# Performance work log

Measured on AMD Instinct MI355X. Metric: run time of the kernel, lower is better.

## Reference

```python
import jax, jax.numpy as jnp
import numpy as np

# Grid config derived from module constants:
# point_cloud_range=[0,-25.6,-2,51.2,25.6,4.4], occ_size=[256,256,32], lss_downsample=[2,2,2]
DX = jnp.array([0.4, 0.4, 0.4], dtype=jnp.float32)
BX = jnp.array([0.2, -25.4, -1.8], dtype=jnp.float32)
NX = (128, 128, 16)  # (x, y, z) voxel counts


def setup_inputs() -> dict:
    key = jax.random.key(0)
    k1, k2, k3 = jax.random.split(key, 3)
    B, N, D, H, W, C = 2, 1, 40, 64, 128, 64  # fH=grd_h//4, fW=grd_w//4, D=40 depth bins
    img_feats = jax.random.normal(k1, (B * N, C, H, W), dtype=jnp.float32)
    depth_logits = jax.random.normal(k2, (B * N, D, H, W), dtype=jnp.float32)
    lo = jnp.array([0.0, -25.6, -2.0], dtype=jnp.float32)
    hi = jnp.array([51.2, 25.6, 4.4], dtype=jnp.float32)
    u = jax.random.uniform(k3, (B, N, D, H, W, 3), dtype=jnp.float32)
    geom = lo + u * (hi - lo)  # ego-frame 3D points of each frustum cell
    return {"img_feats": img_feats, "depth_logits": depth_logits, "geom": geom}


def reference(img_feats, depth_logits, geom):
    B, N, D, H, W, _ = geom.shape
    C = img_feats.shape[1]
    nx_x, nx_y, nx_z = NX

    # ---- LSS lift: depth-distribution-weighted outer product ----
    depth = jax.nn.softmax(depth_logits, axis=1)               # [BN, D, H, W]
    lifted = depth[:, None] * img_feats[:, :, None]            # [BN, C, D, H, W]
    x = lifted.reshape(B, N, C, D, H, W).transpose(0, 1, 3, 4, 5, 2)  # [B,N,D,H,W,C]

    # ---- voxel pooling (splat): scatter-add into BEV/3D grid ----
    Nprime = B * N * D * H * W
    xf = x.reshape(Nprime, C)
    coords = jnp.floor((geom.reshape(Nprime, 3) - (BX - DX / 2.0)) / DX).astype(jnp.int32)
    batch_ix = jnp.repeat(jnp.arange(B, dtype=jnp.int32), N * D * H * W)

    nx_arr = jnp.array(NX, dtype=jnp.int32)
    kept = jnp.all((coords >= 0) & (coords < nx_arr), axis=1)  # in-grid mask

    # linear index: ((b*Z + z)*X + x)*Y + y  -> grid layout [B, Z, X, Y]
    lin = ((batch_ix * nx_z + coords[:, 2]) * nx_x + coords[:, 0]) * nx_y + coords[:, 1]
    lin = jnp.where(kept, lin, 0)
    xf = jnp.where(kept[:, None], xf, 0.0)

    pooled = jax.ops.segment_sum(xf, lin, num_segments=B * nx_z * nx_x * nx_y)  # [B*Z*X*Y, C]

    # final grid [B, C, Z, X, Y]; cat(unbind(dim=2), 1) -> [B, Z*C, X, Y]
    final = pooled.reshape(B, nx_z, nx_x, nx_y, C).transpose(0, 1, 4, 2, 3)  # [B, Z, C, X, Y]
    out = final.reshape(B, nx_z * C, nx_x, nx_y)
    return out
```

## Files before the change

kernel.cpp:

```cpp
#include <hip/hip_runtime.h>
#include <cstddef>

#define BB 2
#define NN 1
#define DD 40
#define HH 64
#define WW 128
#define CC 64
#define GX 128
#define GY 128
#define GZ 16
#define XY (GX * GY)
#define VOX (BB * GZ * GX * GY)
#define KSLOT 16

__global__ __launch_bounds__(256) void lss_tfeat(
    const float* __restrict__ img, float* __restrict__ featT,
    uint4* __restrict__ count4) {
  __shared__ float tile[64][65];
  const int bn = blockIdx.x >> 7;
  const int p0 = (blockIdx.x & 127) << 6;
  const int t = threadIdx.x;

  {
    int base = blockIdx.x * 512 + t;
    count4[base] = make_uint4(0, 0, 0, 0);
    count4[base + 256] = make_uint4(0, 0, 0, 0);
  }

  const float* src = img + (size_t)bn * CC * (HH * WW);
#pragma unroll
  for (int i = 0; i < 4; ++i) {
    int idx = i * 256 + t;
    int r = idx >> 4;
    int c4 = idx & 15;
    float4 v = *(const float4*)(src + (size_t)r * (HH * WW) + p0 + c4 * 4);
    tile[r][c4 * 4 + 0] = v.x;
    tile[r][c4 * 4 + 1] = v.y;
    tile[r][c4 * 4 + 2] = v.z;
    tile[r][c4 * 4 + 3] = v.w;
  }
  __syncthreads();
  float* dst = featT + ((size_t)bn * (HH * WW) + p0) * CC;
#pragma unroll
  for (int i = 0; i < 4; ++i) {
    int idx = i * 256 + t;
    int p = idx >> 4;
    int q = idx & 15;
    float4 v;
    v.x = tile[q * 4 + 0][p];
    v.y = tile[q * 4 + 1][p];
    v.z = tile[q * 4 + 2][p];
    v.w = tile[q * 4 + 3][p];
    *(float4*)(dst + (size_t)p * CC + q * 4) = v;
  }
}

__global__ __launch_bounds__(64) void lss_bin(
    const float* __restrict__ logits, const float* __restrict__ geom,
    unsigned int* __restrict__ count, uint2* __restrict__ rec) {
  const int t = threadIdx.x;
  const int pix = blockIdx.x * 64 + t;
  const int w = pix & (WW - 1);
  const int h = (pix >> 7) & (HH - 1);
  const int bn = pix >> 13;

  float lg[DD];
  const float* lp = logits + ((size_t)bn * DD * HH + h) * WW + w;
#pragma unroll
  for (int d = 0; d < DD; ++d) lg[d] = lp[(size_t)d * (HH * WW)];

  float m = lg[0];
#pragma unroll
  for (int d = 1; d < DD; ++d) m = fmaxf(m, lg[d]);
  float s = 0.0f;
#pragma unroll
  for (int d = 0; d < DD; ++d) {
    lg[d] = __expf(lg[d] - m);
    s += lg[d];
  }
  const float inv = 1.0f / s;

  const float* gp = geom + ((size_t)(bn * DD * HH + h) * WW + w) * 3;
#pragma unroll 8
  for (int d = 0; d < DD; ++d) {
    const size_t gb = (size_t)d * (HH * WW * 3);
    float gx = gp[gb + 0];
    float gy = gp[gb + 1];
    float gz = gp[gb + 2];
    int cx = (int)floorf((gx - 0.0f) / 0.4f);
    int cy = (int)floorf((gy + 25.6f) / 0.4f);
    int cz = (int)floorf((gz + 2.0f) / 0.4f);
    if (cx >= 0 && cx < GX && cy >= 0 && cy < GY && cz >= 0 && cz < GZ) {
      int b = bn / NN;
      int v = ((b * GZ + cz) * GX + cx) * GY + cy;
      unsigned int slot = atomicAdd(&count[v], 1u);
      if (slot < KSLOT)
        rec[(size_t)slot * VOX + v] =
            make_uint2((unsigned)pix, __float_as_uint(lg[d] * inv));
    }
  }
}

__global__ __launch_bounds__(256) void lss_gather(
    const unsigned int* __restrict__ count, const uint2* __restrict__ rec,
    const float* __restrict__ featT, float* __restrict__ out) {
  __shared__ float accs[CC][65];
  __shared__ uint2 recs[KSLOT][64];
  __shared__ unsigned int cnts[64];
  const int t = threadIdx.x;
  const int v0 = blockIdx.x << 6;

  if (t < 64) {
    unsigned int c = count[v0 + t];
    cnts[t] = c > KSLOT ? KSLOT : c;
  }
  __syncthreads();

  {
    const int y = t & 63;
    const int cn = (int)cnts[y];
    for (int s = (t >> 6); s < KSLOT; s += 4)
      if (s < cn) recs[s][y] = rec[(size_t)s * VOX + v0 + y];
  }
  __syncthreads();

  const int lane = t & 63;
  const int wid = t >> 6;
  const int y0 = wid * 16;

  float a[16];
  int cn[16];
#pragma unroll
  for (int i = 0; i < 16; ++i) {
    a[i] = 0.0f;
    cn[i] = (int)cnts[y0 + i];
  }
  int maxcn = 0;
#pragma unroll
  for (int i = 0; i < 16; ++i) maxcn = cn[i] > maxcn ? cn[i] : maxcn;

  for (int s = 0; s < maxcn; ++s) {
    float f[16], w[16];
#pragma unroll
    for (int i = 0; i < 16; ++i) {
      if (s < cn[i]) {
        uint2 r = recs[s][y0 + i];
        w[i] = __uint_as_float(r.y);
        f[i] = featT[(size_t)r.x * CC + lane];
      }
    }
#pragma unroll
    for (int i = 0; i < 16; ++i)
      if (s < cn[i]) a[i] += w[i] * f[i];
  }

#pragma unroll
  for (int i = 0; i < 16; ++i) accs[lane][y0 + i] = a[i];
  __syncthreads();

  const int slab = v0 >> 14;
  const int xy = v0 & (XY - 1);
#pragma unroll
  for (int pass = 0; pass < 4; ++pass) {
    const int c = pass * 16 + (t >> 4);
    const int q = t & 15;
    float4 v;
    v.x = accs[c][q * 4 + 0];
    v.y = accs[c][q * 4 + 1];
    v.z = accs[c][q * 4 + 2];
    v.w = accs[c][q * 4 + 3];
    *(float4*)(out + ((size_t)slab * CC + c) * XY + xy + q * 4) = v;
  }
}

__global__ __launch_bounds__(256) void lss_scatter_direct(
    const float* __restrict__ img, const float* __restrict__ logits,
    const float* __restrict__ geom, float* __restrict__ acc) {
  const int gtid = blockIdx.x * blockDim.x + threadIdx.x;
  const int pix = gtid >> 6;
  const int lane = threadIdx.x & 63;
  if (pix >= BB * NN * HH * WW) return;
  const int w = pix & (WW - 1);
  const int h = (pix >> 7) & (HH - 1);
  const int bn = pix >> 13;

  float logit = -3.0e38f;
  if (lane < DD) logit = logits[((bn * DD + lane) * HH + h) * WW + w];
  float m = logit;
#pragma unroll
  for (int off = 32; off > 0; off >>= 1) m = fmaxf(m, __shfl_xor(m, off));
  float e = (lane < DD) ? __expf(logit - m) : 0.0f;
  float s = e;
#pragma unroll
  for (int off = 32; off > 0; off >>= 1) s += __shfl_xor(s, off);
  const float dep = e / s;

  int base = -1;
  if (lane < DD) {
    size_t gb = ((size_t)((bn * DD + lane) * HH + h) * WW + w) * 3;
    float fx = (geom[gb + 0] - 0.0f) / 0.4f;
    float fy = (geom[gb + 1] + 25.6f) / 0.4f;
    float fz = (geom[gb + 2] + 2.0f) / 0.4f;
    int cx = (int)floorf(fx);
    int cy = (int)floorf(fy);
    int cz = (int)floorf(fz);
    if (cx >= 0 && cx < GX && cy >= 0 && cy < GY && cz >= 0 && cz < GZ) {
      int b = bn / NN;
      base = ((b * GZ + cz) * CC) * XY + cx * GY + cy;
    }
  }
  const float feat = img[((bn * CC + lane) * HH + h) * WW + w];
  for (int d = 0; d < DD; ++d) {
    int bd = __shfl(base, d);
    if (bd >= 0) {
      float wd = __shfl(dep, d);
      atomicAdd(&acc[bd + lane * XY], wd * feat);
    }
  }
}

extern "C" void kernel_launch(void* const* d_in, const int* in_sizes, int n_in,
                              void* d_out, int out_size, void* d_ws, size_t ws_size,
                              hipStream_t stream) {
  const float* img = (const float*)d_in[0];
  const float* logits = (const float*)d_in[1];
  const float* geom = (const float*)d_in[2];
  float* out = (float*)d_out;

  const size_t countBytes = (size_t)VOX * sizeof(unsigned int);
  const size_t recBytes = (size_t)KSLOT * VOX * sizeof(uint2);
  const size_t featTBytes = (size_t)BB * NN * HH * WW * CC * sizeof(float);
  const size_t need = countBytes + recBytes + featTBytes;

  const int pixels = BB * NN * HH * WW;

  if (ws_size >= need) {
    unsigned int* count = (unsigned int*)d_ws;
    uint2* rec = (uint2*)((char*)d_ws + countBytes);
    float* featT = (float*)((char*)d_ws + countBytes + recBytes);

    lss_tfeat<<<BB * NN * (HH * WW / 64), 256, 0, stream>>>(img, featT, (uint4*)count);
    lss_bin<<<pixels / 64, 64, 0, stream>>>(logits, geom, count, rec);
    lss_gather<<<VOX / 64, 256, 0, stream>>>(count, rec, featT, out);
  } else {
    hipMemsetAsync(out, 0, (size_t)BB * GZ * XY * CC * sizeof(float), stream);
    lss_scatter_direct<<<(pixels * 64 + 255) / 256, 256, 0, stream>>>(img, logits, geom, out);
  }
}
```

Before: 247.2 us.

## Split binning into softmax-stats kernel and per-point scatter kernel

Replaces the per-pixel binning kernel, which looped serially over 40 depth bins with only 256 blocks of 64 threads, with two kernels. The first computes the per-pixel softmax max and reciprocal sum; the second assigns one thread per frustum point to compute the weight, the voxel index and the atomic slot insertion. This exposes far more parallelism and coalesces the geom and logits reads. In exchange it adds a kernel launch, a small stats buffer, and re-reads the logits and recomputes the exponentials.

```diff
diff --git a/kernel.cpp b/kernel.cpp
--- a/kernel.cpp
+++ b/kernel.cpp
@@ -11,6 +11,7 @@
 #define GY 128
 #define GZ 16
 #define XY (GX * GY)
+#define HW (HH * WW)
 #define VOX (BB * GZ * GX * GY)
 #define KSLOT 16
 
@@ -28,20 +29,20 @@
     count4[base + 256] = make_uint4(0, 0, 0, 0);
   }
 
-  const float* src = img + (size_t)bn * CC * (HH * WW);
+  const float* src = img + (size_t)bn * CC * HW;
 #pragma unroll
   for (int i = 0; i < 4; ++i) {
     int idx = i * 256 + t;
     int r = idx >> 4;
     int c4 = idx & 15;
-    float4 v = *(const float4*)(src + (size_t)r * (HH * WW) + p0 + c4 * 4);
+    float4 v = *(const float4*)(src + (size_t)r * HW + p0 + c4 * 4);
     tile[r][c4 * 4 + 0] = v.x;
     tile[r][c4 * 4 + 1] = v.y;
     tile[r][c4 * 4 + 2] = v.z;
     tile[r][c4 * 4 + 3] = v.w;
   }
   __syncthreads();
-  float* dst = featT + ((size_t)bn * (HH * WW) + p0) * CC;
+  float* dst = featT + ((size_t)bn * HW + p0) * CC;
 #pragma unroll
   for (int i = 0; i < 4; ++i) {
     int idx = i * 256 + t;
@@ -56,49 +57,54 @@
   }
 }
 
-__global__ __launch_bounds__(64) void lss_bin(
-    const float* __restrict__ logits, const float* __restrict__ geom,
-    unsigned int* __restrict__ count, uint2* __restrict__ rec) {
-  const int t = threadIdx.x;
-  const int pix = blockIdx.x * 64 + t;
-  const int w = pix & (WW - 1);
-  const int h = (pix >> 7) & (HH - 1);
+__global__ __launch_bounds__(256) void lss_rowstats(
+    const float* __restrict__ logits, float2* __restrict__ stats) {
+  const int pix = blockIdx.x * 256 + threadIdx.x;
+  const int hw = pix & (HW - 1);
   const int bn = pix >> 13;
 
   float lg[DD];
-  const float* lp = logits + ((size_t)bn * DD * HH + h) * WW + w;
-#pragma unroll
-  for (int d = 0; d < DD; ++d) lg[d] = lp[(size_t)d * (HH * WW)];
+  const float* lp = logits + (size_t)bn * DD * HW + hw;
+#pragma unroll
+  for (int d = 0; d < DD; ++d) lg[d] = lp[(size_t)d * HW];
 
   float m = lg[0];
 #pragma unroll
   for (int d = 1; d < DD; ++d) m = fmaxf(m, lg[d]);
   float s = 0.0f;
 #pragma unroll
-  for (int d = 0; d < DD; ++d) {
-    lg[d] = __expf(lg[d] - m);
-    s += lg[d];
-  }
-  const float inv = 1.0f / s;
-
-  const float* gp = geom + ((size_t)(bn * DD * HH + h) * WW + w) * 3;
-#pragma unroll 8
-  for (int d = 0; d < DD; ++d) {
-    const size_t gb = (size_t)d * (HH * WW * 3);
-    float gx = gp[gb + 0];
-    float gy = gp[gb + 1];
-    float gz = gp[gb + 2];
-    int cx = (int)floorf((gx - 0.0f) / 0.4f);
-    int cy = (int)floorf((gy + 25.6f) / 0.4f);
-    int cz = (int)floorf((gz + 2.0f) / 0.4f);
-    if (cx >= 0 && cx < GX && cy >= 0 && cy < GY && cz >= 0 && cz < GZ) {
-      int b = bn / NN;
-      int v = ((b * GZ + cz) * GX + cx) * GY + cy;
-      unsigned int slot = atomicAdd(&count[v], 1u);
-      if (slot < KSLOT)
-        rec[(size_t)slot * VOX + v] =
-            make_uint2((unsigned)pix, __float_as_uint(lg[d] * inv));
-    }
+  for (int d = 0; d < DD; ++d) s += __expf(lg[d] - m);
+  stats[pix] = make_float2(m, 1.0f / s);
+}
+
+__global__ __launch_bounds__(256) void lss_scatterbin(
+    const float* __restrict__ logits, const float* __restrict__ geom,
+    const float2* __restrict__ stats,
+    unsigned int* __restrict__ count, uint2* __restrict__ rec) {
+  const int tid = blockIdx.x * 256 + threadIdx.x;
+  const int hw = tid & (HW - 1);
+  const int dbn = tid >> 13;
+  const int bn = dbn / DD;
+  const int pix = bn * HW + hw;
+
+  const float lg = logits[tid];
+  const float2 st = stats[pix];
+  const float wgt = __expf(lg - st.x) * st.y;
+
+  const size_t gb = (size_t)tid * 3;
+  const float gx = geom[gb + 0];
+  const float gy = geom[gb + 1];
+  const float gz = geom[gb + 2];
+  const int cx = (int)floorf((gx - 0.0f) / 0.4f);
+  const int cy = (int)floorf((gy + 25.6f) / 0.4f);
+  const int cz = (int)floorf((gz + 2.0f) / 0.4f);
+  if (cx >= 0 && cx < GX && cy >= 0 && cy < GY && cz >= 0 && cz < GZ) {
+    const int b = bn / NN;
+    const int v = ((b * GZ + cz) * GX + cx) * GY + cy;
+    unsigned int slot = atomicAdd(&count[v], 1u);
+    if (slot < KSLOT)
+      rec[(size_t)slot * VOX + v] =
+          make_uint2((unsigned)pix, __float_as_uint(wgt));
   }
 }
 
@@ -230,18 +236,22 @@
 
   const size_t countBytes = (size_t)VOX * sizeof(unsigned int);
   const size_t recBytes = (size_t)KSLOT * VOX * sizeof(uint2);
-  const size_t featTBytes = (size_t)BB * NN * HH * WW * CC * sizeof(float);
-  const size_t need = countBytes + recBytes + featTBytes;
-
-  const int pixels = BB * NN * HH * WW;
+  const size_t featTBytes = (size_t)BB * NN * HW * CC * sizeof(float);
+  const size_t statsBytes = (size_t)BB * NN * HW * sizeof(float2);
+  const size_t need = countBytes + recBytes + featTBytes + statsBytes;
+
+  const int pixels = BB * NN * HW;
+  const int points = BB * NN * DD * HW;
 
   if (ws_size >= need) {
     unsigned int* count = (unsigned int*)d_ws;
     uint2* rec = (uint2*)((char*)d_ws + countBytes);
     float* featT = (float*)((char*)d_ws + countBytes + recBytes);
-
-    lss_tfeat<<<BB * NN * (HH * WW / 64), 256, 0, stream>>>(img, featT, (uint4*)count);
-    lss_bin<<<pixels / 64, 64, 0, stream>>>(logits, geom, count, rec);
+    float2* stats = (float2*)((char*)d_ws + countBytes + recBytes + featTBytes);
+
+    lss_tfeat<<<BB * NN * (HW / 64), 256, 0, stream>>>(img, featT, (uint4*)count);
+    lss_rowstats<<<pixels / 256, 256, 0, stream>>>(logits, stats);
+    lss_scatterbin<<<points / 256, 256, 0, stream>>>(logits, geom, stats, count, rec);
     lss_gather<<<VOX / 64, 256, 0, stream>>>(count, rec, featT, out);
   } else {
     hipMemsetAsync(out, 0, (size_t)BB * GZ * XY * CC * sizeof(float), stream);
```

Measured after the change: 213.2 us. 1.16x faster.
